# Kernel tuning notes

Measured on AMD Instinct MI355X. Metric: run time of the kernel, lower is better.

Reference implementation:

```python
import jax, jax.numpy as jnp
import numpy as np

D_MODEL = 1024
HEAD_SIZE = 64

def setup_inputs() -> dict:
    key = jax.random.key(0)
    ks = jax.random.split(key, 7)
    s = 1.0 / np.sqrt(D_MODEL)
    x = jax.random.normal(ks[0], (4, 4096, D_MODEL), dtype=jnp.float32)
    Wq = jax.random.uniform(ks[1], (D_MODEL, HEAD_SIZE), jnp.float32, -s, s)
    bq = jax.random.uniform(ks[2], (HEAD_SIZE,), jnp.float32, -s, s)
    Wk = jax.random.uniform(ks[3], (D_MODEL, HEAD_SIZE), jnp.float32, -s, s)
    bk = jax.random.uniform(ks[4], (HEAD_SIZE,), jnp.float32, -s, s)
    Wv = jax.random.uniform(ks[5], (D_MODEL, HEAD_SIZE), jnp.float32, -s, s)
    bv = jax.random.uniform(ks[6], (HEAD_SIZE,), jnp.float32, -s, s)
    return {"x": x, "Wq": Wq, "bq": bq, "Wk": Wk, "bk": bk, "Wv": Wv, "bv": bv}

def reference(x, Wq, bq, Wk, bk, Wv, bv):
    # x: [B, S, D]; projections to [B, S, H]
    Q = jnp.einsum('bsd,dh->bsh', x, Wq) + bq
    K = jnp.einsum('bsd,dh->bsh', x, Wk) + bk
    V = jnp.einsum('bsd,dh->bsh', x, Wv) + bv
    scores = jnp.einsum('bqh,bkh->bqk', Q, K) / jnp.sqrt(jnp.float32(HEAD_SIZE))
    attn = jax.nn.softmax(scores, axis=-1)  # [B, S, S]
    return jnp.einsum('bqk,bkh->bqh', attn, V)
```

## Files before the change

### kernel.cpp

```cpp
#include <hip/hip_runtime.h>
#include <hip/hip_bf16.h>


#define S_LEN 4096
#define D_MODEL 1024

typedef __attribute__((ext_vector_type(8))) short bf16x8;
typedef __attribute__((ext_vector_type(4))) float f32x4;
typedef __attribute__((ext_vector_type(16))) float f32x16;

__device__ inline short f2bf(float f) {
    union { float f; unsigned u; } v;
    v.f = f;
    unsigned r = v.u + 0x7fffu + ((v.u >> 16) & 1u);
    return (short)(r >> 16);
}

__device__ inline unsigned cvt_pk(float lo, float hi) {
    unsigned r;
    asm("v_cvt_pk_bf16_f32 %0, %1, %2" : "=v"(r) : "v"(lo), "v"(hi));
    return r;
}

__device__ inline void pl32swap(unsigned& a, unsigned& b) {
    asm("v_permlane32_swap_b32 %0, %1" : "+v"(a), "+v"(b));
}

__device__ inline f32x16 fzero16() {
    f32x16 z;
#pragma unroll
    for (int i = 0; i < 16; ++i) z[i] = 0.f;
    return z;
}

__device__ inline void gload_lds16(const void* g, void* l) {
    __builtin_amdgcn_global_load_lds((const __attribute__((address_space(1))) void*)g,
                                     (__attribute__((address_space(3))) void*)l, 16, 0, 0);
}

__global__ void prep_w(const float* __restrict__ Wq, const float* __restrict__ Wk,
                       const float* __restrict__ Wv, short* __restrict__ Wt) {
    __shared__ short tile[64][72];
    int mat = blockIdx.x >> 4, kt = blockIdx.x & 15;
    const float* W = (mat == 0) ? Wq : (mat == 1 ? Wk : Wv);
    int tid = threadIdx.x;
    int h = tid & 63, kg = tid >> 6;
#pragma unroll
    for (int i = 0; i < 16; ++i) {
        int kl = kg * 16 + i;
        tile[h][kl] = f2bf(W[(size_t)(kt * 64 + kl) * 64 + h]);
    }
    __syncthreads();
    int h2 = tid >> 2, c = tid & 3;
    bf16x8 v0 = *(const bf16x8*)&tile[h2][c * 16];
    bf16x8 v1 = *(const bf16x8*)&tile[h2][c * 16 + 8];
    short* dst = Wt + (size_t)(mat * 64 + h2) * D_MODEL + kt * 64 + c * 16;
    *(bf16x8*)dst = v0;
    *(bf16x8*)(dst + 8) = v1;
}

__launch_bounds__(256)
__global__ void proj_kernel(const float* __restrict__ x, const short* __restrict__ Wt,
                            const float* __restrict__ bq, const float* __restrict__ bk,
                            const float* __restrict__ bv,
                            short* __restrict__ Qb, short* __restrict__ Kb,
                            short* __restrict__ Vt) {
    __shared__ __align__(16) char bsm[2 * 24576];
    __shared__ short vsm[64][40];
    const float CEXP = 0.18033688011112042f;
    int w = threadIdx.x >> 6;
    int lane = threadIdx.x & 63;
    int g = lane >> 4, ln = lane & 15;
    int rt = w >> 1, nh = w & 1;
    int rowbase = blockIdx.x * 32;

    const char* WtB = (const char*)Wt;

    auto stageW = [&](int buf, int bkt) {
#pragma unroll
        for (int i = 0; i < 6; ++i) {
            int od = w * 6144 + i * 1024 + lane * 16;
            int row = od >> 7, colb = od & 127;
            const char* src = WtB + (size_t)row * 2048 + bkt * 128 + (colb ^ ((row & 7) << 4));
            gload_lds16(src, bsm + buf * 24576 + w * 6144 + i * 1024);
        }
    };

    f32x4 acc[6];
#pragma unroll
    for (int i = 0; i < 6; ++i) acc[i] = (f32x4){0.f, 0.f, 0.f, 0.f};

    const float* xw = x + (size_t)(rowbase + rt * 16 + ln) * D_MODEL + g * 8;

    auto compute = [&](const char* bs, const f32x4& X0, const f32x4& X1,
                       const f32x4& X2, const f32x4& X3) {
        {
            union { bf16x8 v; unsigned u[4]; } A;
            A.u[0] = cvt_pk(X0[0], X0[1]);
            A.u[1] = cvt_pk(X0[2], X0[3]);
            A.u[2] = cvt_pk(X1[0], X1[1]);
            A.u[3] = cvt_pk(X1[2], X1[3]);
#pragma unroll
            for (int nt = 0; nt < 6; ++nt) {
                int row = nh * 96 + nt * 16 + ln;
                bf16x8 bfr = *(const bf16x8*)(bs + row * 128 + ((g * 16) ^ ((row & 7) << 4)));
                acc[nt] = __builtin_amdgcn_mfma_f32_16x16x32_bf16(A.v, bfr, acc[nt], 0, 0, 0);
            }
        }
        {
            union { bf16x8 v; unsigned u[4]; } A;
            A.u[0] = cvt_pk(X2[0], X2[1]);
            A.u[1] = cvt_pk(X2[2], X2[3]);
            A.u[2] = cvt_pk(X3[0], X3[1]);
            A.u[3] = cvt_pk(X3[2], X3[3]);
#pragma unroll
            for (int nt = 0; nt < 6; ++nt) {
                int row = nh * 96 + nt * 16 + ln;
                bf16x8 bfr = *(const bf16x8*)(bs + row * 128 + ((64 + g * 16) ^ ((row & 7) << 4)));
                acc[nt] = __builtin_amdgcn_mfma_f32_16x16x32_bf16(A.v, bfr, acc[nt], 0, 0, 0);
            }
        }
    };

    stageW(0, 0);
    f32x4 XA0 = *(const f32x4*)(xw);
    f32x4 XA1 = *(const f32x4*)(xw + 4);
    f32x4 XA2 = *(const f32x4*)(xw + 32);
    f32x4 XA3 = *(const f32x4*)(xw + 36);
    f32x4 XB0 = *(const f32x4*)(xw + 64);
    f32x4 XB1 = *(const f32x4*)(xw + 68);
    f32x4 XB2 = *(const f32x4*)(xw + 96);
    f32x4 XB3 = *(const f32x4*)(xw + 100);

#pragma unroll 1
    for (int bk2 = 0; bk2 < 16; bk2 += 2) {
        asm volatile("s_waitcnt vmcnt(4)" ::: "memory");
        __builtin_amdgcn_s_barrier();
        __builtin_amdgcn_sched_barrier(0);
        {
            int nt1 = bk2 + 1 > 15 ? 15 : bk2 + 1;
            stageW((bk2 + 1) & 1, nt1);
        }
        compute(bsm + (bk2 & 1) * 24576, XA0, XA1, XA2, XA3);
        {
            int nx = bk2 + 2 > 15 ? 15 : bk2 + 2;
            const float* xn = xw + nx * 64;
            XA0 = *(const f32x4*)(xn);
            XA1 = *(const f32x4*)(xn + 4);
            XA2 = *(const f32x4*)(xn + 32);
            XA3 = *(const f32x4*)(xn + 36);
        }
        asm volatile("s_waitcnt vmcnt(4)" ::: "memory");
        __builtin_amdgcn_s_barrier();
        __builtin_amdgcn_sched_barrier(0);
        {
            int nt2 = bk2 + 2 > 15 ? 15 : bk2 + 2;
            stageW(bk2 & 1, nt2);
        }
        compute(bsm + ((bk2 + 1) & 1) * 24576, XB0, XB1, XB2, XB3);
        {
            int nx = bk2 + 3 > 15 ? 15 : bk2 + 3;
            const float* xn = xw + nx * 64;
            XB0 = *(const f32x4*)(xn);
            XB1 = *(const f32x4*)(xn + 4);
            XB2 = *(const f32x4*)(xn + 32);
            XB3 = *(const f32x4*)(xn + 36);
        }
    }

#pragma unroll
    for (int nt = 0; nt < 6; ++nt) {
        int c = nh * 96 + nt * 16 + ln;
        int proj = c >> 6;
        int h = c & 63;
        float bias = (proj == 0 ? bq : (proj == 1 ? bk : bv))[h];
#pragma unroll
        for (int r = 0; r < 4; ++r) {
            int srow = rowbase + rt * 16 + g * 4 + r;
            float v = acc[nt][r] + bias;
            if (proj == 0) v *= CEXP;
            short hv = f2bf(v);
            if (proj == 0) {
                Qb[(size_t)srow * 64 + h] = hv;
            } else if (proj == 1) {
                Kb[(size_t)srow * 64 + h] = hv;
            } else {
                vsm[h][rt * 16 + g * 4 + r] = hv;
            }
        }
    }
    __syncthreads();
    {
        int t = threadIdx.x;
        int h = t >> 2, c = t & 3;
        bf16x8 val = *(const bf16x8*)&vsm[h][c * 8];
        int bb = rowbase >> 12;
        int sg = (rowbase & 4095) + c * 8;
        *(bf16x8*)(Vt + ((size_t)(bb * 64 + h) << 12) + sg) = val;
    }
}

__launch_bounds__(512)
__global__ void attn_kernel(const short* __restrict__ Qb, const short* __restrict__ Kb,
                            const short* __restrict__ Vt, float* __restrict__ out) {
    __shared__ __align__(16) char smraw[131072];
    __shared__ float lsm[256];
    int lane = threadIdx.x & 63;
    int w = threadIdx.x >> 6;
    int l31 = lane & 31, hi = lane >> 5;
    int sp = w >> 1, qt = w & 1;

    int bid = blockIdx.x;
    int sb = (bid & 7) * 32 + (bid >> 3);
    int b = sb >> 6, qs = sb & 63;
    size_t qrow0 = ((size_t)b << 12) + (size_t)qs * 64;

    char* base = smraw + sp * 32768;
    char* kbuf = base;
    char* vbuf = base + 16384;

    const char* KB = (const char*)(Kb + (((size_t)b << 12) + sp * 1024) * 64);
    const char* VB = (const char*)Vt + (((size_t)b * 64) << 13) + (size_t)sp * 2048;

    auto stageT = [&](int buf, int t) {
        if (qt == 0) {
            char* dst = kbuf + buf * 8192;
#pragma unroll
            for (int i = 0; i < 8; ++i) {
                int od = i * 1024 + lane * 16;
                int row = od >> 7, colb = od & 127;
                const char* src = KB + (size_t)(t * 64 + row) * 128 + (colb ^ ((row & 7) << 4));
                gload_lds16(src, dst + i * 1024);
            }
        } else {
            char* dst = vbuf + buf * 8192;
#pragma unroll
            for (int i = 0; i < 8; ++i) {
                int od = i * 1024 + lane * 16;
                int row = od >> 7, colb = od & 127;
                const char* src = VB + (size_t)row * 8192 + t * 128 + (colb ^ ((row & 7) << 4));
                gload_lds16(src, dst + i * 1024);
            }
        }
    };

    bf16x8 qf[4];
    {
        const short* qp = Qb + (qrow0 + qt * 32 + l31) * 64 + hi * 8;
#pragma unroll
        for (int ks = 0; ks < 4; ++ks) qf[ks] = *(const bf16x8*)(qp + ks * 16);
    }

    f32x16 oacc0 = fzero16(), oacc1 = fzero16();
    float lacc[16];
#pragma unroll
    for (int r = 0; r < 16; ++r) lacc[r] = 0.f;

    int swz = (l31 & 7) << 4;
    stageT(0, 0);

#pragma unroll 1
    for (int t = 0; t < 16; ++t) {
        asm volatile("s_waitcnt vmcnt(0)" ::: "memory");
        __builtin_amdgcn_s_barrier();
        __builtin_amdgcn_sched_barrier(0);
        if (t < 15) stageT((t + 1) & 1, t + 1);

        const char* kc = kbuf + (t & 1) * 8192;
        const char* vc = vbuf + (t & 1) * 8192;

        bf16x8 kf[8];
#pragma unroll
        for (int kt = 0; kt < 2; ++kt)
#pragma unroll
            for (int ks = 0; ks < 4; ++ks)
                kf[kt * 4 + ks] = *(const bf16x8*)(kc + (kt * 32 + l31) * 128
                                                  + ((ks * 32 + hi * 16) ^ swz));
        f32x16 s0 = fzero16(), s1 = fzero16();
#pragma unroll
        for (int ks = 0; ks < 4; ++ks) {
            s0 = __builtin_amdgcn_mfma_f32_32x32x16_bf16(kf[ks], qf[ks], s0, 0, 0, 0);
            s1 = __builtin_amdgcn_mfma_f32_32x32x16_bf16(kf[4 + ks], qf[ks], s1, 0, 0, 0);
        }

        bf16x8 vf[8];
#pragma unroll
        for (int ht = 0; ht < 2; ++ht)
#pragma unroll
            for (int kk = 0; kk < 4; ++kk)
                vf[ht * 4 + kk] = *(const bf16x8*)(vc + (ht * 32 + l31) * 128
                                                   + ((kk * 32 + hi * 16) ^ swz));

        float p0[16], p1[16];
#pragma unroll
        for (int r = 0; r < 16; ++r) p0[r] = exp2f(s0[r]);
#pragma unroll
        for (int r = 0; r < 16; ++r) p1[r] = exp2f(s1[r]);
#pragma unroll
        for (int r = 0; r < 16; ++r) lacc[r] += p0[r] + p1[r];

        union { unsigned u[4]; bf16x8 v; } t00, t01, t10, t11;
        {
            unsigned D[8];
#pragma unroll
            for (int dw = 0; dw < 8; ++dw) D[dw] = cvt_pk(p0[2 * dw], p0[2 * dw + 1]);
            pl32swap(D[0], D[2]); pl32swap(D[1], D[3]);
            pl32swap(D[4], D[6]); pl32swap(D[5], D[7]);
            t00.u[0] = D[0]; t00.u[1] = D[1]; t00.u[2] = D[2]; t00.u[3] = D[3];
            t01.u[0] = D[4]; t01.u[1] = D[5]; t01.u[2] = D[6]; t01.u[3] = D[7];
        }
        {
            unsigned D[8];
#pragma unroll
            for (int dw = 0; dw < 8; ++dw) D[dw] = cvt_pk(p1[2 * dw], p1[2 * dw + 1]);
            pl32swap(D[0], D[2]); pl32swap(D[1], D[3]);
            pl32swap(D[4], D[6]); pl32swap(D[5], D[7]);
            t10.u[0] = D[0]; t10.u[1] = D[1]; t10.u[2] = D[2]; t10.u[3] = D[3];
            t11.u[0] = D[4]; t11.u[1] = D[5]; t11.u[2] = D[6]; t11.u[3] = D[7];
        }

        oacc0 = __builtin_amdgcn_mfma_f32_32x32x16_bf16(vf[0], t00.v, oacc0, 0, 0, 0);
        oacc1 = __builtin_amdgcn_mfma_f32_32x32x16_bf16(vf[4], t00.v, oacc1, 0, 0, 0);
        oacc0 = __builtin_amdgcn_mfma_f32_32x32x16_bf16(vf[1], t01.v, oacc0, 0, 0, 0);
        oacc1 = __builtin_amdgcn_mfma_f32_32x32x16_bf16(vf[5], t01.v, oacc1, 0, 0, 0);
        oacc0 = __builtin_amdgcn_mfma_f32_32x32x16_bf16(vf[2], t10.v, oacc0, 0, 0, 0);
        oacc1 = __builtin_amdgcn_mfma_f32_32x32x16_bf16(vf[6], t10.v, oacc1, 0, 0, 0);
        oacc0 = __builtin_amdgcn_mfma_f32_32x32x16_bf16(vf[3], t11.v, oacc0, 0, 0, 0);
        oacc1 = __builtin_amdgcn_mfma_f32_32x32x16_bf16(vf[7], t11.v, oacc1, 0, 0, 0);
    }

    float lfin;
    {
        float lt[8];
#pragma unroll
        for (int r = 0; r < 8; ++r) lt[r] = lacc[r] + lacc[r + 8];
#pragma unroll
        for (int st = 4; st >= 1; st >>= 1)
#pragma unroll
            for (int r = 0; r < 4; ++r)
                if (r < st) lt[r] += lt[r + st];
        lfin = lt[0] + __shfl_xor(lt[0], 32);
    }

    __syncthreads();
    float* osm = (float*)smraw;
    {
        float* ow = osm + (size_t)(w * 32 + l31) * 68;
#pragma unroll
        for (int r = 0; r < 16; ++r) {
            int h = (r & 3) + 8 * (r >> 2) + 4 * hi;
            ow[h] = oacc0[r];
            ow[32 + h] = oacc1[r];
        }
        if (hi == 0) lsm[w * 32 + l31] = lfin;
    }
    __syncthreads();
    {
        int tq = threadIdx.x >> 3, hb = (threadIdx.x & 7) * 8;
        int qt2 = tq >> 5, ql = tq & 31;
        f32x4 oa = (f32x4){0.f, 0.f, 0.f, 0.f}, ob = (f32x4){0.f, 0.f, 0.f, 0.f};
        float lsum = 0.f;
#pragma unroll
        for (int sp2 = 0; sp2 < 4; ++sp2) {
            int w2 = sp2 * 2 + qt2;
            lsum += lsm[w2 * 32 + ql];
            const float* src = osm + (size_t)(w2 * 32 + ql) * 68 + hb;
            f32x4 x0 = *(const f32x4*)src;
            f32x4 x1 = *(const f32x4*)(src + 4);
#pragma unroll
            for (int j = 0; j < 4; ++j) { oa[j] += x0[j]; ob[j] += x1[j]; }
        }
        float inv = 1.f / lsum;
        f32x4 r0, r1;
#pragma unroll
        for (int j = 0; j < 4; ++j) { r0[j] = oa[j] * inv; r1[j] = ob[j] * inv; }
        float* op = out + (qrow0 + tq) * 64 + hb;
        *(f32x4*)op = r0;
        *(f32x4*)(op + 4) = r1;
    }
}

extern "C" void kernel_launch(void* const* d_in, const int* in_sizes, int n_in,
                              void* d_out, int out_size, void* d_ws, size_t ws_size,
                              hipStream_t stream) {
    const float* x  = (const float*)d_in[0];
    const float* Wq = (const float*)d_in[1];
    const float* bq = (const float*)d_in[2];
    const float* Wk = (const float*)d_in[3];
    const float* bk = (const float*)d_in[4];
    const float* Wv = (const float*)d_in[5];
    const float* bv = (const float*)d_in[6];

    short* ws = (short*)d_ws;
    short* Wt = ws;
    short* Qb = Wt + 192 * 1024;
    short* Kb = Qb + 16384 * 64;
    short* Vt = Kb + 16384 * 64;

    prep_w<<<48, 256, 0, stream>>>(Wq, Wk, Wv, Wt);
    proj_kernel<<<512, 256, 0, stream>>>(x, Wt, bq, bk, bv, Qb, Kb, Vt);
    attn_kernel<<<256, 512, 0, stream>>>(Qb, Kb, Vt, (float*)d_out);
}
```

Before: 68.82 us.

## Pre-swizzle weights into MFMA fragment order and load B directly to registers

The weight prep kernel now writes bf16 weights in the exact per-lane MFMA B-fragment layout. The projection kernel loads these fragments straight from global memory into registers with double-buffered register arrays, replacing the LDS staging, XOR swizzle and per-step barriers. This removes LDS traffic and block synchronisation, but adds register pressure (24 bf16x8 fragments per thread) and relies on L2/cache hits because every wave now reads the weights redundantly.

```diff
diff --git a/kernel.cpp b/kernel.cpp
--- a/kernel.cpp
+++ b/kernel.cpp
@@ -39,33 +39,25 @@
 }
 
 __global__ void prep_w(const float* __restrict__ Wq, const float* __restrict__ Wk,
-                       const float* __restrict__ Wv, short* __restrict__ Wt) {
-    __shared__ short tile[64][72];
-    int mat = blockIdx.x >> 4, kt = blockIdx.x & 15;
-    const float* W = (mat == 0) ? Wq : (mat == 1 ? Wk : Wv);
-    int tid = threadIdx.x;
-    int h = tid & 63, kg = tid >> 6;
-#pragma unroll
-    for (int i = 0; i < 16; ++i) {
-        int kl = kg * 16 + i;
-        tile[h][kl] = f2bf(W[(size_t)(kt * 64 + kl) * 64 + h]);
-    }
-    __syncthreads();
-    int h2 = tid >> 2, c = tid & 3;
-    bf16x8 v0 = *(const bf16x8*)&tile[h2][c * 16];
-    bf16x8 v1 = *(const bf16x8*)&tile[h2][c * 16 + 8];
-    short* dst = Wt + (size_t)(mat * 64 + h2) * D_MODEL + kt * 64 + c * 16;
-    *(bf16x8*)dst = v0;
-    *(bf16x8*)(dst + 8) = v1;
+                       const float* __restrict__ Wv, short* __restrict__ WtF) {
+    int idx = blockIdx.x * 256 + threadIdx.x;
+    int j = idx & 7;
+    int lane = (idx >> 3) & 63;
+    int f = idx >> 9;
+    int ntg = f % 12;
+    int kb = f / 12;
+    int k = (kb >> 1) * 64 + (kb & 1) * 32 + (lane >> 4) * 8 + j;
+    int c = ntg * 16 + (lane & 15);
+    const float* W = (c < 64) ? Wq : (c < 128 ? Wk : Wv);
+    WtF[idx] = f2bf(W[k * 64 + (c & 63)]);
 }
 
 __launch_bounds__(256)
-__global__ void proj_kernel(const float* __restrict__ x, const short* __restrict__ Wt,
+__global__ void proj_kernel(const float* __restrict__ x, const short* __restrict__ WtF,
                             const float* __restrict__ bq, const float* __restrict__ bk,
                             const float* __restrict__ bv,
                             short* __restrict__ Qb, short* __restrict__ Kb,
                             short* __restrict__ Vt) {
-    __shared__ __align__(16) char bsm[2 * 24576];
     __shared__ short vsm[64][40];
     const float CEXP = 0.18033688011112042f;
     int w = threadIdx.x >> 6;
@@ -74,55 +66,42 @@
     int rt = w >> 1, nh = w & 1;
     int rowbase = blockIdx.x * 32;
 
-    const char* WtB = (const char*)Wt;
-
-    auto stageW = [&](int buf, int bkt) {
-#pragma unroll
-        for (int i = 0; i < 6; ++i) {
-            int od = w * 6144 + i * 1024 + lane * 16;
-            int row = od >> 7, colb = od & 127;
-            const char* src = WtB + (size_t)row * 2048 + bkt * 128 + (colb ^ ((row & 7) << 4));
-            gload_lds16(src, bsm + buf * 24576 + w * 6144 + i * 1024);
-        }
+    f32x4 acc[6];
+#pragma unroll
+    for (int i = 0; i < 6; ++i) acc[i] = (f32x4){0.f, 0.f, 0.f, 0.f};
+
+    const float* xw = x + (size_t)(rowbase + rt * 16 + ln) * D_MODEL + g * 8;
+
+    auto loadF = [&](bf16x8* F, int t) {
+#pragma unroll
+        for (int kk = 0; kk < 2; ++kk)
+#pragma unroll
+            for (int nt = 0; nt < 6; ++nt)
+                F[kk * 6 + nt] = *(const bf16x8*)(WtF
+                    + ((((t * 2 + kk) * 12 + nh * 6 + nt) << 9) + lane * 8));
     };
 
-    f32x4 acc[6];
-#pragma unroll
-    for (int i = 0; i < 6; ++i) acc[i] = (f32x4){0.f, 0.f, 0.f, 0.f};
-
-    const float* xw = x + (size_t)(rowbase + rt * 16 + ln) * D_MODEL + g * 8;
-
-    auto compute = [&](const char* bs, const f32x4& X0, const f32x4& X1,
-                       const f32x4& X2, const f32x4& X3) {
-        {
-            union { bf16x8 v; unsigned u[4]; } A;
-            A.u[0] = cvt_pk(X0[0], X0[1]);
-            A.u[1] = cvt_pk(X0[2], X0[3]);
-            A.u[2] = cvt_pk(X1[0], X1[1]);
-            A.u[3] = cvt_pk(X1[2], X1[3]);
-#pragma unroll
-            for (int nt = 0; nt < 6; ++nt) {
-                int row = nh * 96 + nt * 16 + ln;
-                bf16x8 bfr = *(const bf16x8*)(bs + row * 128 + ((g * 16) ^ ((row & 7) << 4)));
-                acc[nt] = __builtin_amdgcn_mfma_f32_16x16x32_bf16(A.v, bfr, acc[nt], 0, 0, 0);
-            }
-        }
-        {
-            union { bf16x8 v; unsigned u[4]; } A;
-            A.u[0] = cvt_pk(X2[0], X2[1]);
-            A.u[1] = cvt_pk(X2[2], X2[3]);
-            A.u[2] = cvt_pk(X3[0], X3[1]);
-            A.u[3] = cvt_pk(X3[2], X3[3]);
-#pragma unroll
-            for (int nt = 0; nt < 6; ++nt) {
-                int row = nh * 96 + nt * 16 + ln;
-                bf16x8 bfr = *(const bf16x8*)(bs + row * 128 + ((64 + g * 16) ^ ((row & 7) << 4)));
-                acc[nt] = __builtin_amdgcn_mfma_f32_16x16x32_bf16(A.v, bfr, acc[nt], 0, 0, 0);
-            }
-        }
+    auto computeF = [&](const bf16x8* F, const f32x4& X0, const f32x4& X1,
+                        const f32x4& X2, const f32x4& X3) {
+        union { bf16x8 v; unsigned u[4]; } A;
+        A.u[0] = cvt_pk(X0[0], X0[1]);
+        A.u[1] = cvt_pk(X0[2], X0[3]);
+        A.u[2] = cvt_pk(X1[0], X1[1]);
+        A.u[3] = cvt_pk(X1[2], X1[3]);
+#pragma unroll
+        for (int nt = 0; nt < 6; ++nt)
+            acc[nt] = __builtin_amdgcn_mfma_f32_16x16x32_bf16(A.v, F[nt], acc[nt], 0, 0, 0);
+        A.u[0] = cvt_pk(X2[0], X2[1]);
+        A.u[1] = cvt_pk(X2[2], X2[3]);
+        A.u[2] = cvt_pk(X3[0], X3[1]);
+        A.u[3] = cvt_pk(X3[2], X3[3]);
+#pragma unroll
+        for (int nt = 0; nt < 6; ++nt)
+            acc[nt] = __builtin_amdgcn_mfma_f32_16x16x32_bf16(A.v, F[6 + nt], acc[nt], 0, 0, 0);
     };
 
-    stageW(0, 0);
+    bf16x8 Fa[12], Fb[12];
+    loadF(Fa, 0);
     f32x4 XA0 = *(const f32x4*)(xw);
     f32x4 XA1 = *(const f32x4*)(xw + 4);
     f32x4 XA2 = *(const f32x4*)(xw + 32);
@@ -133,33 +112,21 @@
     f32x4 XB3 = *(const f32x4*)(xw + 100);
 
 #pragma unroll 1
-    for (int bk2 = 0; bk2 < 16; bk2 += 2) {
-        asm volatile("s_waitcnt vmcnt(4)" ::: "memory");
-        __builtin_amdgcn_s_barrier();
-        __builtin_amdgcn_sched_barrier(0);
+    for (int t = 0; t < 16; t += 2) {
+        loadF(Fb, t + 1 > 15 ? 15 : t + 1);
+        computeF(Fa, XA0, XA1, XA2, XA3);
         {
-            int nt1 = bk2 + 1 > 15 ? 15 : bk2 + 1;
-            stageW((bk2 + 1) & 1, nt1);
-        }
-        compute(bsm + (bk2 & 1) * 24576, XA0, XA1, XA2, XA3);
-        {
-            int nx = bk2 + 2 > 15 ? 15 : bk2 + 2;
+            int nx = t + 2 > 15 ? 15 : t + 2;
             const float* xn = xw + nx * 64;
             XA0 = *(const f32x4*)(xn);
             XA1 = *(const f32x4*)(xn + 4);
             XA2 = *(const f32x4*)(xn + 32);
             XA3 = *(const f32x4*)(xn + 36);
         }
-        asm volatile("s_waitcnt vmcnt(4)" ::: "memory");
-        __builtin_amdgcn_s_barrier();
-        __builtin_amdgcn_sched_barrier(0);
+        loadF(Fa, t + 2 > 15 ? 15 : t + 2);
+        computeF(Fb, XB0, XB1, XB2, XB3);
         {
-            int nt2 = bk2 + 2 > 15 ? 15 : bk2 + 2;
-            stageW(bk2 & 1, nt2);
-        }
-        compute(bsm + ((bk2 + 1) & 1) * 24576, XB0, XB1, XB2, XB3);
-        {
-            int nx = bk2 + 3 > 15 ? 15 : bk2 + 3;
+            int nx = t + 3 > 15 ? 15 : t + 3;
             const float* xn = xw + nx * 64;
             XB0 = *(const f32x4*)(xn);
             XB1 = *(const f32x4*)(xn + 4);
@@ -392,12 +359,12 @@
     const float* bv = (const float*)d_in[6];
 
     short* ws = (short*)d_ws;
-    short* Wt = ws;
-    short* Qb = Wt + 192 * 1024;
+    short* WtF = ws;
+    short* Qb = WtF + 192 * 1024;
     short* Kb = Qb + 16384 * 64;
     short* Vt = Kb + 16384 * 64;
 
-    prep_w<<<48, 256, 0, stream>>>(Wq, Wk, Wv, Wt);
-    proj_kernel<<<512, 256, 0, stream>>>(x, Wt, bq, bk, bv, Qb, Kb, Vt);
+    prep_w<<<768, 256, 0, stream>>>(Wq, Wk, Wv, WtF);
+    proj_kernel<<<512, 256, 0, stream>>>(x, WtF, bq, bk, bv, Qb, Kb, Vt);
     attn_kernel<<<256, 512, 0, stream>>>(Qb, Kb, Vt, (float*)d_out);
 }
```

Measured after the change: 71.67 us. 4.1% more time.
